# Kernel tuning notes

Measured on AMD Instinct MI355X. Metric: run time of the kernel, lower is better.

## Reference

```python
import jax, jax.numpy as jnp
import numpy as np

B, S, D, H = 8, 2048, 512, 512


def setup_inputs() -> dict:
    key = jax.random.key(0)
    ks = jax.random.split(key, 5)
    scale = 0.05
    x = jax.random.normal(ks[0], (B, S, D), dtype=jnp.float32)
    Wq = jax.random.normal(ks[1], (D, H), dtype=jnp.float32) * scale
    Wk = jax.random.normal(ks[2], (D, H), dtype=jnp.float32) * scale
    Wv = jax.random.normal(ks[3], (D, H), dtype=jnp.float32) * scale
    Wo = jax.random.normal(ks[4], (H, D), dtype=jnp.float32) * scale
    bq = jnp.zeros((H,), dtype=jnp.float32)
    bk = jnp.zeros((H,), dtype=jnp.float32)
    bv = jnp.zeros((H,), dtype=jnp.float32)
    bo = jnp.zeros((D,), dtype=jnp.float32)
    return {"x": x, "Wq": Wq, "bq": bq, "Wk": Wk, "bk": bk,
            "Wv": Wv, "bv": bv, "Wo": Wo, "bo": bo}


def reference(x, Wq, bq, Wk, bk, Wv, bv, Wo, bo):
    # x: [B, S, D]
    q = jnp.einsum('bsd,dh->bsh', x, Wq) + bq  # [B,S,H]
    k = jnp.einsum('bsd,dh->bsh', x, Wk) + bk
    v = jnp.einsum('bsd,dh->bsh', x, Wv) + bv
    scores = jnp.einsum('bqh,bkh->bqk', q, k) / jnp.sqrt(jnp.float32(H))  # [B,S,S]
    weights = jax.nn.softmax(scores, axis=-1)
    context = jnp.einsum('bqk,bkh->bqh', weights, v)  # [B,S,H]
    out = jnp.einsum('bsh,hd->bsd', context, Wo) + bo  # [B,S,D]
    return out + x
```

## Files before the change

kernel.cpp:

```cpp
#include <hip/hip_runtime.h>
#include <stdint.h>


typedef __attribute__((ext_vector_type(4))) float f32x4;
typedef __attribute__((ext_vector_type(8))) short short8;
typedef __attribute__((ext_vector_type(4))) unsigned short ushort4v;
typedef __attribute__((ext_vector_type(8))) unsigned short ushort8v;
typedef unsigned short bf16_t;

#define AS1 __attribute__((address_space(1)))
#define AS3 __attribute__((address_space(3)))

static __device__ __forceinline__ unsigned short f2bf(float f) {
  unsigned int u = __float_as_uint(f);
  u += 0x7fffu + ((u >> 16) & 1u);
  return (unsigned short)(u >> 16);
}

__global__ __launch_bounds__(256) void ws_sentinel(float* out) {
  out[threadIdx.x] = 1e30f;
}

__global__ __launch_bounds__(256) void cast_f32_bf16(
    const float* __restrict__ in, bf16_t* __restrict__ out, int n4) {
  int i = blockIdx.x * 256 + threadIdx.x;
  if (i >= n4) return;
  float4 v = ((const float4*)in)[i];
  ushort4v o = { f2bf(v.x), f2bf(v.y), f2bf(v.z), f2bf(v.w) };
  ((ushort4v*)out)[i] = o;
}

__global__ __launch_bounds__(256) void cast_transpose_512(
    const float* __restrict__ in, bf16_t* __restrict__ out) {
  __shared__ float tile[32][33];
  int bx = blockIdx.x * 32;
  int by = blockIdx.y * 32;
  int tx = threadIdx.x & 31;
  int ty = threadIdx.x >> 5;
#pragma unroll
  for (int k = 0; k < 4; ++k)
    tile[ty + k * 8][tx] = in[(by + ty + k * 8) * 512 + bx + tx];
  __syncthreads();
#pragma unroll
  for (int k = 0; k < 4; ++k)
    out[(bx + ty + k * 8) * 512 + by + tx] = f2bf(tile[tx][ty + k * 8]);
}

__global__ __launch_bounds__(256) void concat_bias(
    const float* __restrict__ b0, const float* __restrict__ b1,
    const float* __restrict__ b2, float* __restrict__ out) {
  int i = blockIdx.x * 256 + threadIdx.x;
  const float* src = (i < 512) ? b0 : (i < 1024) ? b1 : b2;
  out[i] = src[i & 511];
}

__global__ __launch_bounds__(256) void transpose_strided(
    const bf16_t* __restrict__ in, long inZ, int inLd,
    bf16_t* __restrict__ out, long outZ, int R, int C) {
  __shared__ bf16_t tile[32][33];
  long ibase = (long)blockIdx.z * inZ;
  long obase = (long)blockIdx.z * outZ;
  int r0 = blockIdx.x * 32, c0 = blockIdx.y * 32;
  int tx = threadIdx.x & 31, ty = threadIdx.x >> 5;
#pragma unroll
  for (int k = 0; k < 4; ++k)
    tile[ty + k * 8][tx] = in[ibase + (long)(r0 + ty + k * 8) * inLd + c0 + tx];
  __syncthreads();
#pragma unroll
  for (int k = 0; k < 4; ++k)
    out[obase + (long)(c0 + ty + k * 8) * R + r0 + tx] = tile[tx][ty + k * 8];
}

template <typename OT>
__global__ __launch_bounds__(256, 2) void gemm_bt(
    const bf16_t* __restrict__ A, int lda, long sA,
    const bf16_t* __restrict__ BT, int ldb, long sB,
    const float* __restrict__ bias, const float* __restrict__ resid,
    OT* __restrict__ Cout, int ldc, long sC, int M, int N, int K, float scale) {
  __shared__ __align__(16) bf16_t As[128 * 64];
  __shared__ __align__(16) bf16_t Bs[128 * 64];
  const int z = blockIdx.z;
  const bf16_t* Ab = A + (long)z * sA;
  const bf16_t* Bb = BT + (long)z * sB;
  const int tile_m = blockIdx.x * 128;
  const int tile_n = blockIdx.y * 128;
  const int t = threadIdx.x;
  const int lane = t & 63;
  const int wave = t >> 6;
  const int wm = (wave >> 1) * 64;
  const int wn = (wave & 1) * 64;

  f32x4 acc[4][4];
#pragma unroll
  for (int i = 0; i < 4; ++i)
#pragma unroll
    for (int j = 0; j < 4; ++j) acc[i][j] = f32x4{0.f, 0.f, 0.f, 0.f};

  const bf16_t* gA[4];
  const bf16_t* gB[4];
  int ldsoff[4];
#pragma unroll
  for (int i = 0; i < 4; ++i) {
    int o16 = i * 256 + t;
    int row = o16 >> 3;
    int slot = (o16 & 7) ^ (row & 7);
    gA[i] = Ab + (long)(tile_m + row) * lda + slot * 8;
    gB[i] = Bb + (long)(tile_n + row) * ldb + slot * 8;
    ldsoff[i] = o16 * 8;
  }

  const int nk = K >> 6;
  for (int kt = 0; kt < nk; ++kt) {
#pragma unroll
    for (int i = 0; i < 4; ++i) {
      __builtin_amdgcn_global_load_lds((const AS1 unsigned int*)(gA[i]),
                                       (AS3 unsigned int*)(&As[ldsoff[i]]),
                                       16, 0, 0);
      __builtin_amdgcn_global_load_lds((const AS1 unsigned int*)(gB[i]),
                                       (AS3 unsigned int*)(&Bs[ldsoff[i]]),
                                       16, 0, 0);
      gA[i] += 64;
      gB[i] += 64;
    }
    __syncthreads();
#pragma unroll
    for (int ks = 0; ks < 2; ++ks) {
      short8 af[4], bfr[4];
#pragma unroll
      for (int i = 0; i < 4; ++i) {
        int ra = wm + i * 16 + (lane & 15);
        int oa = ra * 128 + ((ks * 64 + (lane >> 4) * 16) ^ ((ra & 7) << 4));
        af[i] = *(const short8*)((const char*)As + oa);
        int rb = wn + i * 16 + (lane & 15);
        int ob = rb * 128 + ((ks * 64 + (lane >> 4) * 16) ^ ((rb & 7) << 4));
        bfr[i] = *(const short8*)((const char*)Bs + ob);
      }
#pragma unroll
      for (int i = 0; i < 4; ++i)
#pragma unroll
        for (int j = 0; j < 4; ++j)
          acc[i][j] = __builtin_amdgcn_mfma_f32_16x16x32_bf16(
              af[i], bfr[j], acc[i][j], 0, 0, 0);
    }
    __syncthreads();
  }

  OT* Cz = Cout + (long)z * sC;
#pragma unroll
  for (int i = 0; i < 4; ++i) {
    int crow0 = tile_m + wm + i * 16 + ((lane >> 4) << 2);
#pragma unroll
    for (int j = 0; j < 4; ++j) {
      int ccol = tile_n + wn + j * 16 + (lane & 15);
      float bv = bias ? bias[ccol] : 0.f;
#pragma unroll
      for (int r = 0; r < 4; ++r) {
        long idx = (long)(crow0 + r) * ldc + ccol;
        float val = acc[i][j][r] * scale + bv;
        if (resid) val += resid[idx];
        if constexpr (sizeof(OT) == 2)
          Cz[idx] = (OT)f2bf(val);
        else
          Cz[idx] = (OT)val;
      }
    }
  }
}

__global__ __launch_bounds__(256, 4) void softmax_rows(float* __restrict__ S) {
  long row = blockIdx.x;
  float* srow = S + row * 2048;
  bf16_t* prow = (bf16_t*)srow;
  int t = threadIdx.x;
  float4 a = ((const float4*)srow)[2 * t];
  float4 b = ((const float4*)srow)[2 * t + 1];
  float m = fmaxf(fmaxf(fmaxf(a.x, a.y), fmaxf(a.z, a.w)),
                  fmaxf(fmaxf(b.x, b.y), fmaxf(b.z, b.w)));
#pragma unroll
  for (int off = 32; off; off >>= 1) m = fmaxf(m, __shfl_xor(m, off, 64));
  __shared__ float red[8];
  if ((t & 63) == 0) red[t >> 6] = m;
  __syncthreads();
  m = fmaxf(fmaxf(red[0], red[1]), fmaxf(red[2], red[3]));
  float e0 = __expf(a.x - m), e1 = __expf(a.y - m);
  float e2 = __expf(a.z - m), e3 = __expf(a.w - m);
  float e4 = __expf(b.x - m), e5 = __expf(b.y - m);
  float e6 = __expf(b.z - m), e7 = __expf(b.w - m);
  float s = ((e0 + e1) + (e2 + e3)) + ((e4 + e5) + (e6 + e7));
#pragma unroll
  for (int off = 32; off; off >>= 1) s += __shfl_xor(s, off, 64);
  if ((t & 63) == 0) red[4 + (t >> 6)] = s;
  __syncthreads();
  s = (red[4] + red[5]) + (red[6] + red[7]);
  float inv = 1.0f / s;
  ushort8v o = { f2bf(e0 * inv), f2bf(e1 * inv), f2bf(e2 * inv),
                 f2bf(e3 * inv), f2bf(e4 * inv), f2bf(e5 * inv),
                 f2bf(e6 * inv), f2bf(e7 * inv) };
  *(ushort8v*)(prow + t * 8) = o;
}

extern "C" void kernel_launch(void* const* d_in, const int* in_sizes, int n_in,
                              void* d_out, int out_size, void* d_ws,
                              size_t ws_size, hipStream_t stream) {
  const float* x  = (const float*)d_in[0];
  const float* Wq = (const float*)d_in[1];
  const float* bq = (const float*)d_in[2];
  const float* Wk = (const float*)d_in[3];
  const float* bk = (const float*)d_in[4];
  const float* Wv = (const float*)d_in[5];
  const float* bv = (const float*)d_in[6];
  const float* Wo = (const float*)d_in[7];
  const float* bo = (const float*)d_in[8];
  float* out = (float*)d_out;

  const int S = 2048, D = 512;
  const long MS = 16384;
  const long MB = 1024 * 1024;

  const size_t need = 211 * MB;
  if (ws_size < need) {
    ws_sentinel<<<1, 256, 0, stream>>>(out);
    return;
  }
  char* w = (char*)d_ws;
  bf16_t* xb    = (bf16_t*)(w);
  bf16_t* ctx   = (bf16_t*)(w);
  bf16_t* QKV   = (bf16_t*)(w + 16 * MB);
  bf16_t* VT    = (bf16_t*)(w + 64 * MB);
  float*  Sc    = (float*)(w + 80 * MB);
  bf16_t* WqkvT = (bf16_t*)(w + 208 * MB);
  bf16_t* WoT   = WqkvT + 1536 * 512;
  float*  bqkv  = (float*)(WoT + 512 * 512);

  cast_f32_bf16<<<dim3(8192), 256, 0, stream>>>(x, xb, (int)(MS * D / 4));
  dim3 g512(16, 16);
  cast_transpose_512<<<g512, 256, 0, stream>>>(Wq, WqkvT);
  cast_transpose_512<<<g512, 256, 0, stream>>>(Wk, WqkvT + 512 * 512);
  cast_transpose_512<<<g512, 256, 0, stream>>>(Wv, WqkvT + 2 * 512 * 512);
  cast_transpose_512<<<g512, 256, 0, stream>>>(Wo, WoT);
  concat_bias<<<dim3(6), 256, 0, stream>>>(bq, bk, bv, bqkv);

  gemm_bt<bf16_t><<<dim3(128, 12), 256, 0, stream>>>(
      xb, 512, 0, WqkvT, 512, 0, bqkv, nullptr,
      QKV, 1536, 0, 16384, 1536, 512, 1.0f);

  transpose_strided<<<dim3(64, 16, 8), 256, 0, stream>>>(
      QKV + 1024, (long)S * 1536, 1536, VT, (long)512 * S, S, 512);

  const float rsq = 0.04419417382415922f;
  gemm_bt<float><<<dim3(16, 16, 8), 256, 0, stream>>>(
      QKV, 1536, (long)S * 1536, QKV + 512, 1536, (long)S * 1536,
      nullptr, nullptr, Sc, 2048, (long)S * S, 2048, 2048, 512, rsq);

  softmax_rows<<<dim3(16384), 256, 0, stream>>>(Sc);

  gemm_bt<bf16_t><<<dim3(16, 4, 8), 256, 0, stream>>>(
      (const bf16_t*)Sc, 4096, (long)S * 4096, VT, 2048, (long)512 * S,
      nullptr, nullptr, ctx, 512, (long)S * 512, 2048, 512, 2048, 1.0f);

  gemm_bt<float><<<dim3(128, 4), 256, 0, stream>>>(
      ctx, 512, 0, WoT, 512, 0, bo, x, out, 512, 0, 16384, 512, 512, 1.0f);
}
```

Before: 311.2 us.

## Store attention scores in bf16 and fuse V transpose into QKV GEMM epilogue

The score GEMM now writes bf16 instead of fp32, and softmax reads and writes bf16 in place. This halves the traffic of the large score matrix across the GEMM, the softmax and the PV GEMM. The V transpose kernel is removed; the QKV GEMM epilogue writes V columns directly in transposed layout. The four weight cast-transposes are merged into one launch. In exchange, scores are rounded to bf16 before softmax, which costs precision, and the transposed V stores are scattered rather than coalesced.

```diff
diff --git a/kernel.cpp b/kernel.cpp
--- a/kernel.cpp
+++ b/kernel.cpp
@@ -15,6 +15,9 @@
   unsigned int u = __float_as_uint(f);
   u += 0x7fffu + ((u >> 16) & 1u);
   return (unsigned short)(u >> 16);
+}
+static __device__ __forceinline__ float bf2f(unsigned short h) {
+  return __uint_as_float(((unsigned int)h) << 16);
 }
 
 __global__ __launch_bounds__(256) void ws_sentinel(float* out) {
@@ -30,9 +33,14 @@
   ((ushort4v*)out)[i] = o;
 }
 
-__global__ __launch_bounds__(256) void cast_transpose_512(
-    const float* __restrict__ in, bf16_t* __restrict__ out) {
+__global__ __launch_bounds__(256) void cast_transpose_w(
+    const float* __restrict__ Wq, const float* __restrict__ Wk,
+    const float* __restrict__ Wv, const float* __restrict__ Wo,
+    bf16_t* __restrict__ WqkvT, bf16_t* __restrict__ WoT) {
   __shared__ float tile[32][33];
+  int z = blockIdx.z;
+  const float* in = (z == 0) ? Wq : (z == 1) ? Wk : (z == 2) ? Wv : Wo;
+  bf16_t* out = (z < 3) ? WqkvT + z * 512 * 512 : WoT;
   int bx = blockIdx.x * 32;
   int by = blockIdx.y * 32;
   int tx = threadIdx.x & 31;
@@ -54,28 +62,12 @@
   out[i] = src[i & 511];
 }
 
-__global__ __launch_bounds__(256) void transpose_strided(
-    const bf16_t* __restrict__ in, long inZ, int inLd,
-    bf16_t* __restrict__ out, long outZ, int R, int C) {
-  __shared__ bf16_t tile[32][33];
-  long ibase = (long)blockIdx.z * inZ;
-  long obase = (long)blockIdx.z * outZ;
-  int r0 = blockIdx.x * 32, c0 = blockIdx.y * 32;
-  int tx = threadIdx.x & 31, ty = threadIdx.x >> 5;
-#pragma unroll
-  for (int k = 0; k < 4; ++k)
-    tile[ty + k * 8][tx] = in[ibase + (long)(r0 + ty + k * 8) * inLd + c0 + tx];
-  __syncthreads();
-#pragma unroll
-  for (int k = 0; k < 4; ++k)
-    out[obase + (long)(c0 + ty + k * 8) * R + r0 + tx] = tile[tx][ty + k * 8];
-}
-
 template <typename OT>
 __global__ __launch_bounds__(256, 2) void gemm_bt(
     const bf16_t* __restrict__ A, int lda, long sA,
     const bf16_t* __restrict__ BT, int ldb, long sB,
     const float* __restrict__ bias, const float* __restrict__ resid,
+    bf16_t* __restrict__ vt_out,
     OT* __restrict__ Cout, int ldc, long sC, int M, int N, int K, float scale) {
   __shared__ __align__(16) bf16_t As[128 * 64];
   __shared__ __align__(16) bf16_t Bs[128 * 64];
@@ -153,50 +145,65 @@
     for (int j = 0; j < 4; ++j) {
       int ccol = tile_n + wn + j * 16 + (lane & 15);
       float bv = bias ? bias[ccol] : 0.f;
-#pragma unroll
-      for (int r = 0; r < 4; ++r) {
-        long idx = (long)(crow0 + r) * ldc + ccol;
-        float val = acc[i][j][r] * scale + bv;
-        if (resid) val += resid[idx];
-        if constexpr (sizeof(OT) == 2)
-          Cz[idx] = (OT)f2bf(val);
-        else
-          Cz[idx] = (OT)val;
+      if (vt_out && ccol >= 1024) {
+        int c = ccol - 1024;
+#pragma unroll
+        for (int r = 0; r < 4; ++r) {
+          int rr = crow0 + r;
+          float val = acc[i][j][r] * scale + bv;
+          vt_out[((long)(rr >> 11) << 20) + ((long)c << 11) + (rr & 2047)] =
+              f2bf(val);
+        }
+      } else {
+#pragma unroll
+        for (int r = 0; r < 4; ++r) {
+          long idx = (long)(crow0 + r) * ldc + ccol;
+          float val = acc[i][j][r] * scale + bv;
+          if (resid) val += resid[idx];
+          if constexpr (sizeof(OT) == 2)
+            Cz[idx] = (OT)f2bf(val);
+          else
+            Cz[idx] = (OT)val;
+        }
       }
     }
   }
 }
 
-__global__ __launch_bounds__(256, 4) void softmax_rows(float* __restrict__ S) {
+__global__ __launch_bounds__(256, 4) void softmax_rows_bf16(
+    bf16_t* __restrict__ S) {
   long row = blockIdx.x;
-  float* srow = S + row * 2048;
-  bf16_t* prow = (bf16_t*)srow;
+  bf16_t* srow = S + row * 2048;
   int t = threadIdx.x;
-  float4 a = ((const float4*)srow)[2 * t];
-  float4 b = ((const float4*)srow)[2 * t + 1];
-  float m = fmaxf(fmaxf(fmaxf(a.x, a.y), fmaxf(a.z, a.w)),
-                  fmaxf(fmaxf(b.x, b.y), fmaxf(b.z, b.w)));
+  ushort8v v = *(ushort8v*)(srow + t * 8);
+  float e[8];
+#pragma unroll
+  for (int k = 0; k < 8; ++k) e[k] = bf2f(v[k]);
+  float m = e[0];
+#pragma unroll
+  for (int k = 1; k < 8; ++k) m = fmaxf(m, e[k]);
 #pragma unroll
   for (int off = 32; off; off >>= 1) m = fmaxf(m, __shfl_xor(m, off, 64));
   __shared__ float red[8];
   if ((t & 63) == 0) red[t >> 6] = m;
   __syncthreads();
   m = fmaxf(fmaxf(red[0], red[1]), fmaxf(red[2], red[3]));
-  float e0 = __expf(a.x - m), e1 = __expf(a.y - m);
-  float e2 = __expf(a.z - m), e3 = __expf(a.w - m);
-  float e4 = __expf(b.x - m), e5 = __expf(b.y - m);
-  float e6 = __expf(b.z - m), e7 = __expf(b.w - m);
-  float s = ((e0 + e1) + (e2 + e3)) + ((e4 + e5) + (e6 + e7));
+  float s = 0.f;
+#pragma unroll
+  for (int k = 0; k < 8; ++k) {
+    e[k] = __expf(e[k] - m);
+    s += e[k];
+  }
 #pragma unroll
   for (int off = 32; off; off >>= 1) s += __shfl_xor(s, off, 64);
   if ((t & 63) == 0) red[4 + (t >> 6)] = s;
   __syncthreads();
   s = (red[4] + red[5]) + (red[6] + red[7]);
   float inv = 1.0f / s;
-  ushort8v o = { f2bf(e0 * inv), f2bf(e1 * inv), f2bf(e2 * inv),
-                 f2bf(e3 * inv), f2bf(e4 * inv), f2bf(e5 * inv),
-                 f2bf(e6 * inv), f2bf(e7 * inv) };
-  *(ushort8v*)(prow + t * 8) = o;
+  ushort8v o;
+#pragma unroll
+  for (int k = 0; k < 8; ++k) o[k] = f2bf(e[k] * inv);
+  *(ushort8v*)(srow + t * 8) = o;
 }
 
 extern "C" void kernel_launch(void* const* d_in, const int* in_sizes, int n_in,
@@ -217,7 +224,7 @@
   const long MS = 16384;
   const long MB = 1024 * 1024;
 
-  const size_t need = 211 * MB;
+  const size_t need = 147 * MB;
   if (ws_size < need) {
     ws_sentinel<<<1, 256, 0, stream>>>(out);
     return;
@@ -227,37 +234,33 @@
   bf16_t* ctx   = (bf16_t*)(w);
   bf16_t* QKV   = (bf16_t*)(w + 16 * MB);
   bf16_t* VT    = (bf16_t*)(w + 64 * MB);
-  float*  Sc    = (float*)(w + 80 * MB);
-  bf16_t* WqkvT = (bf16_t*)(w + 208 * MB);
+  bf16_t* Sc    = (bf16_t*)(w + 80 * MB);
+  bf16_t* WqkvT = (bf16_t*)(w + 144 * MB);
   bf16_t* WoT   = WqkvT + 1536 * 512;
   float*  bqkv  = (float*)(WoT + 512 * 512);
 
   cast_f32_bf16<<<dim3(8192), 256, 0, stream>>>(x, xb, (int)(MS * D / 4));
-  dim3 g512(16, 16);
-  cast_transpose_512<<<g512, 256, 0, stream>>>(Wq, WqkvT);
-  cast_transpose_512<<<g512, 256, 0, stream>>>(Wk, WqkvT + 512 * 512);
-  cast_transpose_512<<<g512, 256, 0, stream>>>(Wv, WqkvT + 2 * 512 * 512);
-  cast_transpose_512<<<g512, 256, 0, stream>>>(Wo, WoT);
+  cast_transpose_w<<<dim3(16, 16, 4), 256, 0, stream>>>(Wq, Wk, Wv, Wo,
+                                                        WqkvT, WoT);
   concat_bias<<<dim3(6), 256, 0, stream>>>(bq, bk, bv, bqkv);
 
   gemm_bt<bf16_t><<<dim3(128, 12), 256, 0, stream>>>(
-      xb, 512, 0, WqkvT, 512, 0, bqkv, nullptr,
+      xb, 512, 0, WqkvT, 512, 0, bqkv, nullptr, VT,
       QKV, 1536, 0, 16384, 1536, 512, 1.0f);
 
-  transpose_strided<<<dim3(64, 16, 8), 256, 0, stream>>>(
-      QKV + 1024, (long)S * 1536, 1536, VT, (long)512 * S, S, 512);
-
   const float rsq = 0.04419417382415922f;
-  gemm_bt<float><<<dim3(16, 16, 8), 256, 0, stream>>>(
+  gemm_bt<bf16_t><<<dim3(16, 16, 8), 256, 0, stream>>>(
       QKV, 1536, (long)S * 1536, QKV + 512, 1536, (long)S * 1536,
-      nullptr, nullptr, Sc, 2048, (long)S * S, 2048, 2048, 512, rsq);
-
-  softmax_rows<<<dim3(16384), 256, 0, stream>>>(Sc);
+      nullptr, nullptr, nullptr, Sc, 2048, (long)S * S, 2048, 2048, 512, rsq);
+
+  softmax_rows_bf16<<<dim3(16384), 256, 0, stream>>>(Sc);
 
   gemm_bt<bf16_t><<<dim3(16, 4, 8), 256, 0, stream>>>(
-      (const bf16_t*)Sc, 4096, (long)S * 4096, VT, 2048, (long)512 * S,
-      nullptr, nullptr, ctx, 512, (long)S * 512, 2048, 512, 2048, 1.0f);
+      Sc, 2048, (long)S * 2048, VT, 2048, (long)512 * S,
+      nullptr, nullptr, nullptr, ctx, 512, (long)S * 512, 2048, 512, 2048,
+      1.0f);
 
   gemm_bt<float><<<dim3(128, 4), 256, 0, stream>>>(
-      ctx, 512, 0, WoT, 512, 0, bo, x, out, 512, 0, 16384, 512, 512, 1.0f);
-}
+      ctx, 512, 0, WoT, 512, 0, bo, x, nullptr, out, 512, 0,
+      16384, 512, 512, 1.0f);
+}
```

Result: faster. 290.3 us (-6.7%).
